# Performance work log

Hardware: AMD Instinct MI355X
Metric: run time of the kernel (lower is better)

Reference implementation:

```python
import jax, jax.numpy as jnp
import numpy as np

B, L, E, A, H = 1024, 200, 128, 128, 4

def setup_inputs() -> dict:
    key = jax.random.key(0)
    k1, k2, k3, k4, k5, k6 = jax.random.split(key, 6)
    inp = jax.random.normal(k1, (B, L, E), dtype=jnp.float32)
    mask = jax.random.randint(k2, (B, L), 0, 2).astype(bool)
    # guarantee at least one valid position per row (realistic: histories are non-empty)
    mask = mask.at[:, 0].set(True)
    pos_enc = jax.random.normal(k3, (1, L, E), dtype=jnp.float32)
    W1 = jax.random.normal(k4, (E, A), dtype=jnp.float32) / np.sqrt(E)
    W2 = jax.random.normal(k5, (A, H), dtype=jnp.float32) / np.sqrt(A)
    W_out = jax.random.normal(k6, (H * E, E), dtype=jnp.float32) / np.sqrt(H * E)
    return {"input": inp, "mask": mask, "pos_enc": pos_enc, "W1": W1, "W2": W2, "W_out": W_out}

def reference(input, mask, pos_enc, W1, W2, W_out):
    fm = mask.astype(input.dtype)[..., None]          # [B, L, 1]
    x = input * fm                                     # zero out padded positions
    xp = x + pos_enc                                   # broadcast [1, L, E]
    hidden = jnp.tanh(xp @ W1)                         # [B, L, A]
    att = hidden @ W2                                  # [B, L, H]
    att = jnp.swapaxes(att, 1, 2)                      # [B, H, L]
    neg = jnp.asarray(-(2.0 ** 32) + 1.0, dtype=att.dtype)
    att = jnp.where(mask[:, None, :], att, neg)
    att = jax.nn.softmax(att, axis=-1)                 # [B, H, L]
    pooled = jnp.einsum('bhl,ble->bhe', att, x)        # [B, H, E]
    flat = pooled.reshape(pooled.shape[0], -1)         # [B, H*E]
    return flat @ W_out                                # [B, E]
```

## Files before the change

kernel.cpp:

```cpp
#include <hip/hip_runtime.h>
#include <cfloat>

#define Bn 1024
#define Ln 200
#define En 128
#define An 128
#define Hn 4

#define WS_POSW1   0
#define WS_W1FRAG  106496
#define WS_ATTPOOL 139264
#define SLOT       1664
#define WS_WOUTT   1843200
#define WS_NEEDED  1974272

using f32x4  = __attribute__((ext_vector_type(4))) float;
using bf16x8 = __attribute__((ext_vector_type(8))) short;

__device__ __forceinline__ unsigned short f2bf(float f){
    unsigned u = __builtin_bit_cast(unsigned, f);
    u = (u + 0x7FFFu + ((u >> 16) & 1u)) >> 16;
    return (unsigned short)u;
}
__device__ __forceinline__ float bf2f(unsigned short s){
    unsigned u = ((unsigned)s) << 16;
    return __builtin_bit_cast(float, u);
}
__device__ __forceinline__ float tanh_cheap(float x){
    float e = __expf(2.f * x);
    float r = __builtin_amdgcn_rcpf(e + 1.f);
    return fmaf(-2.f, r, 1.f);
}
__device__ __forceinline__ float tanh_fast(float x){
    x = fminf(fmaxf(x, -12.f), 12.f);
    float e = __expf(2.f * x);
    return 1.f - 2.f / (e + 1.f);
}
__device__ __forceinline__ unsigned cvt_pk_bf16(float lo, float hi){
    unsigned r;
    asm("v_cvt_pk_bf16_f32 %0, %1, %2" : "=v"(r) : "v"(lo), "v"(hi));
    return r;
}
__device__ __forceinline__ int swz(int row, int k){
    return row * 128 + ((((k >> 3) ^ (row & 15)) << 3) | (k & 7));
}

__global__ __launch_bounds__(256) void sap_prep(
    const float* __restrict__ pos, const float* __restrict__ W1,
    const float* __restrict__ Wout, void* __restrict__ ws)
{
    const int t = threadIdx.x, blk = blockIdx.x;
    if (blk < 104){
        float* posW1 = (float*)((char*)ws + WS_POSW1);
        int l = blk * 2 + (t >> 7), a = t & 127;
        float acc = 0.f;
        if (l < Ln){
            #pragma unroll 4
            for (int k = 0; k < 128; ++k)
                acc += pos[l * En + k] * W1[k * An + a];
        }
        posW1[l * An + a] = acc;
    } else if (blk < 106){
        unsigned short* w1f = (unsigned short*)((char*)ws + WS_W1FRAG);
        int s = (blk - 104) * 256 + t;
        int lane = s & 63;
        int A = s >> 6;
        int c = lane & 15, q = lane >> 4;
        #pragma unroll
        for (int ks = 0; ks < 4; ++ks){
            unsigned short v[8];
            #pragma unroll
            for (int j = 0; j < 8; ++j)
                v[j] = f2bf(W1[(ks * 32 + q * 8 + j) * An + A * 16 + c]);
            *(bf16x8*)&w1f[(s * 4 + ks) * 8] = *(bf16x8*)v;
        }
    } else {
        unsigned short* wt = (unsigned short*)((char*)ws + WS_WOUTT);
        int flat = ((blk - 106) * 256 + t) * 4;
        int e = flat >> 9, k = flat & 511;
        unsigned short v[4];
        #pragma unroll
        for (int i = 0; i < 4; ++i)
            v[i] = f2bf(Wout[(size_t)(k + i) * En + e]);
        *(uint2*)&wt[flat] = *(uint2*)v;
    }
}

__global__ __launch_bounds__(512, 4) void sap_att10(
    const float* __restrict__ inp, const void* __restrict__ maskp,
    const float* __restrict__ W2, void* __restrict__ ws)
{
    __shared__ __align__(16) char smem_u[32768];
    __shared__ float s_att4[208 * 4];
    __shared__ float s_mask[256];

    unsigned short* s_x = (unsigned short*)smem_u;
    float (*s_part)[4][64] = (float (*)[4][64])(smem_u + 16384);
    float (*s_scr)[512]    = (float (*)[512])smem_u;

    const int t = threadIdx.x, lane = t & 63, w = t >> 6;
    const int c = lane & 15, q = lane >> 4;
    const int b = blockIdx.x;

    const unsigned short* w1f   = (const unsigned short*)((char*)ws + WS_W1FRAG);
    const float*          posW1 = (const float*)((char*)ws + WS_POSW1);
    unsigned short*       slot  = (unsigned short*)((char*)ws + WS_ATTPOOL + (size_t)b * SLOT);

    bf16x8 af[4];
    #pragma unroll
    for (int ks = 0; ks < 4; ++ks)
        af[ks] = *(const bf16x8*)&w1f[((w * 64 + lane) * 4 + ks) * 8];
    float4 w2a[4];
    #pragma unroll
    for (int v = 0; v < 4; ++v)
        w2a[v] = *(const float4*)&W2[(w * 16 + q * 4 + v) * Hn];

    {
        unsigned word = ((const unsigned*)maskp)[lane];
        unsigned long long bi  = __ballot(word > 1u);
        unsigned long long bfm = __ballot(word != 0u && word != 0x3F800000u);
        int flag = (bi == 0ull) ? 0 : ((bfm == 0ull) ? 2 : 1);
        if (t < 256){
            float m = 0.f;
            if (t < Ln){
                int mv;
                if (flag == 0)      mv = ((const int*)maskp)[b * Ln + t] != 0;
                else if (flag == 1) mv = ((const unsigned char*)maskp)[b * Ln + t] != 0;
                else                mv = ((const float*)maskp)[b * Ln + t] != 0.f;
                m = mv ? 1.f : 0.f;
            }
            s_mask[t] = m;
        }
    }

    for (int cch = 0; cch < 4; ++cch){
        const int NT = (cch < 3) ? 4 : 1;

        {
            const float4* in4 = (const float4*)(inp + (size_t)b * (Ln * En) + cch * 64 * En);
            #define PUTV(vi, idx) { int ll = (idx) >> 5, kk = ((idx) & 31) * 4;            \
                uint2 val = make_uint2(cvt_pk_bf16(vi.x, vi.y), cvt_pk_bf16(vi.z, vi.w));  \
                *(uint2*)&s_x[swz(ll, kk)] = val; }
            if (cch < 3){
                float4 u0 = in4[t], u1 = in4[t + 512], u2 = in4[t + 1024], u3 = in4[t + 1536];
                PUTV(u0, t) PUTV(u1, t + 512) PUTV(u2, t + 1024) PUTV(u3, t + 1536)
            } else {
                uint2 val = make_uint2(0u, 0u);
                if (t < 256){
                    float4 u0 = in4[t];
                    val = make_uint2(cvt_pk_bf16(u0.x, u0.y), cvt_pk_bf16(u0.z, u0.w));
                }
                int ll = t >> 5, kk = (t & 31) * 4;
                *(uint2*)&s_x[swz(ll, kk)] = val;
            }
            #undef PUTV
        }
        __syncthreads();

        for (int lt = 0; lt < NT; ++lt){
            int brow = lt * 16 + c;
            bf16x8 bfr[4];
            #pragma unroll
            for (int ks = 0; ks < 4; ++ks){
                int g = (ks * 4 + q) ^ c;
                bfr[ks] = *(bf16x8*)&s_x[brow * 128 + (g << 3)];
            }
            f32x4 acc = *(const f32x4*)&posW1[(size_t)(cch * 64 + brow) * An + w * 16 + q * 4];
            #pragma unroll
            for (int ks = 0; ks < 4; ++ks)
                acc = __builtin_amdgcn_mfma_f32_16x16x32_bf16(af[ks], bfr[ks], acc, 0, 0, 0);
            float contrib[4] = {0.f, 0.f, 0.f, 0.f};
            #pragma unroll
            for (int v = 0; v < 4; ++v){
                float hv = tanh_cheap(acc[v]);
                contrib[0] += hv * w2a[v].x;
                contrib[1] += hv * w2a[v].y;
                contrib[2] += hv * w2a[v].z;
                contrib[3] += hv * w2a[v].w;
            }
            #pragma unroll
            for (int h = 0; h < 4; ++h){
                contrib[h] += __shfl_xor(contrib[h], 16, 64);
                contrib[h] += __shfl_xor(contrib[h], 32, 64);
            }
            s_part[w][q][lt * 16 + c] = contrib[q];
        }
        __syncthreads();

        if (t < 256){
            int h = t >> 6, l = t & 63, gl = cch * 64 + l;
            if (gl < Ln){
                float a = 0.f;
                #pragma unroll
                for (int w2 = 0; w2 < 8; ++w2) a += s_part[w2][h][l];
                s_att4[gl * 4 + h] = (s_mask[gl] > 0.5f) ? a : -1.0e30f;
            }
        }
    }
    __syncthreads();

    if (t < 256){
        const int h = t >> 6, sl = t & 63;
        float v[4]; float mx = -FLT_MAX;
        #pragma unroll
        for (int i = 0; i < 4; ++i){
            int l = sl + i * 64;
            v[i] = (l < Ln) ? s_att4[l * 4 + h] : -3.0e38f;
            mx = fmaxf(mx, v[i]);
        }
        for (int s = 32; s; s >>= 1) mx = fmaxf(mx, __shfl_xor(mx, s, 64));
        float e[4]; float sum = 0.f;
        #pragma unroll
        for (int i = 0; i < 4; ++i){
            int l = sl + i * 64;
            e[i] = (l < Ln) ? __expf(v[i] - mx) : 0.f;
            sum += e[i];
        }
        for (int s = 32; s; s >>= 1) sum += __shfl_xor(sum, s, 64);
        float inv = 1.f / sum;
        #pragma unroll
        for (int i = 0; i < 4; ++i){
            int l = sl + i * 64;
            if (l < Ln) s_att4[l * 4 + h] = e[i] * inv;
        }
    }
    __syncthreads();

    {
        const int eg = t & 31, r = t >> 5;
        const float* xin = inp + (size_t)b * (Ln * En);
        f32x4 a0 = {0.f,0.f,0.f,0.f}, a1 = a0, a2 = a0, a3 = a0;
        for (int i = 0; i < 13; ++i){
            int l = i * 16 + r;
            if (l < Ln){
                f32x4 xv = *(const f32x4*)&xin[l * En + eg * 4];
                f32x4 w4 = *(const f32x4*)&s_att4[l * 4];
                a0 += xv * w4[0];
                a1 += xv * w4[1];
                a2 += xv * w4[2];
                a3 += xv * w4[3];
            }
        }
        *(f32x4*)&s_scr[r][0 * 128 + eg * 4] = a0;
        *(f32x4*)&s_scr[r][1 * 128 + eg * 4] = a1;
        *(f32x4*)&s_scr[r][2 * 128 + eg * 4] = a2;
        *(f32x4*)&s_scr[r][3 * 128 + eg * 4] = a3;
    }
    __syncthreads();

    {
        float sum = 0.f;
        #pragma unroll
        for (int r2 = 0; r2 < 16; ++r2) sum += s_scr[r2][t];
        slot[t] = f2bf(sum);
    }
}

__global__ __launch_bounds__(256) void sap_out(
    const void* __restrict__ ws, float* __restrict__ out)
{
    const unsigned short* wt = (const unsigned short*)((const char*)ws + WS_WOUTT);
    const int t = threadIdx.x, lane = t & 63, w = t >> 6;
    const int c = lane & 15, q = lane >> 4;
    const int b0 = blockIdx.x * 16;
    const int e0 = (blockIdx.y * 4 + w) * 16;

    const unsigned short* pslot =
        (const unsigned short*)((const char*)ws + WS_ATTPOOL + (size_t)(b0 + c) * SLOT);

    f32x4 acc = {0.f, 0.f, 0.f, 0.f};
    #pragma unroll 4
    for (int ks = 0; ks < 16; ++ks){
        bf16x8 afr = *(const bf16x8*)&pslot[ks * 32 + q * 8];
        bf16x8 bfr = *(const bf16x8*)&wt[(e0 + c) * 512 + ks * 32 + q * 8];
        acc = __builtin_amdgcn_mfma_f32_16x16x32_bf16(afr, bfr, acc, 0, 0, 0);
    }
    #pragma unroll
    for (int v = 0; v < 4; ++v)
        out[(size_t)(b0 + q * 4 + v) * En + e0 + c] = acc[v];
}

__global__ __launch_bounds__(512, 4) void sap_fused_v2(
    const float* __restrict__ inp, const void* __restrict__ maskp,
    const float* __restrict__ pos, const float* __restrict__ W1,
    const float* __restrict__ W2, const float* __restrict__ Wout,
    float* __restrict__ out)
{
#define LP 208
    __shared__ unsigned short s_xp [LP * 128];
    __shared__ float s_att [4 * LP];
    __shared__ float s_mask[LP];
    __shared__ float s_pool[512];
    __shared__ float s_red [512];
    __shared__ int   s_flag;

    const int t = threadIdx.x;
    const int b = blockIdx.x;
    const int lane = t & 63, w = t >> 6;
    const int c = lane & 15, q = lane >> 4;

    if (t == 0){
        const unsigned* mw = (const unsigned*)maskp;
        int fi = 1, ff = 1;
        for (int i = 0; i < 64; ++i){
            unsigned word = mw[i];
            if (word > 1u) fi = 0;
            if (word != 0u && word != 0x3F800000u) ff = 0;
        }
        s_flag = fi ? 0 : (ff ? 2 : 1);
    }
    bf16x8 af[4];
    {
        const int arow = w * 16 + c;
        #pragma unroll
        for (int ks = 0; ks < 4; ++ks)
            #pragma unroll
            for (int j = 0; j < 8; ++j)
                af[ks][j] = (short)f2bf(W1[(ks * 32 + q * 8 + j) * An + arow]);
    }
    float w2a[4][4];
    #pragma unroll
    for (int v = 0; v < 4; ++v){
        float4 wv = *(const float4*)&W2[(w * 16 + q * 4 + v) * Hn];
        w2a[v][0] = wv.x; w2a[v][1] = wv.y; w2a[v][2] = wv.z; w2a[v][3] = wv.w;
    }
    __syncthreads();
    const int flag = s_flag;
    for (int l = t; l < LP; l += 512){
        float m = 0.f;
        if (l < Ln){
            int mv;
            if (flag == 0)      mv = ((const int*)maskp)[b * Ln + l] != 0;
            else if (flag == 1) mv = ((const unsigned char*)maskp)[b * Ln + l] != 0;
            else                mv = ((const float*)maskp)[b * Ln + l] != 0.f;
            m = mv ? 1.f : 0.f;
        }
        s_mask[l] = m;
    }
    for (int i = t; i < 4 * LP; i += 512) s_att[i] = 0.f;
    __syncthreads();
    {
        const float4* in4 = (const float4*)(inp + (size_t)b * (Ln * En));
        const float4* p4  = (const float4*)pos;
        #pragma unroll
        for (int it = 0; it < 13; ++it){
            int idx = it * 512 + t;
            int l = idx >> 5;
            int k = (idx & 31) * 4;
            uint2 val;
            if (idx < 6400){
                float m = s_mask[l];
                float4 a = in4[idx];
                float4 p = p4[idx];
                val = make_uint2((unsigned)f2bf(a.x*m+p.x) | ((unsigned)f2bf(a.y*m+p.y) << 16),
                                 (unsigned)f2bf(a.z*m+p.z) | ((unsigned)f2bf(a.w*m+p.w) << 16));
            } else val = make_uint2(0u, 0u);
            *(uint2*)&s_xp[swz(l, k)] = val;
        }
    }
    __syncthreads();
    for (int lt = 0; lt < 13; ++lt){
        int brow = lt * 16 + c;
        bf16x8 bfr[4];
        #pragma unroll
        for (int ks = 0; ks < 4; ++ks){
            int g = (ks * 4 + q) ^ c;
            bfr[ks] = *(bf16x8*)&s_xp[brow * 128 + (g << 3)];
        }
        f32x4 acc = {0.f, 0.f, 0.f, 0.f};
        #pragma unroll
        for (int ks = 0; ks < 4; ++ks)
            acc = __builtin_amdgcn_mfma_f32_16x16x32_bf16(af[ks], bfr[ks], acc, 0, 0, 0);
        float hv[4];
        #pragma unroll
        for (int v = 0; v < 4; ++v) hv[v] = tanh_fast(acc[v]);
        #pragma unroll
        for (int h = 0; h < 4; ++h){
            float contrib = hv[0]*w2a[0][h] + hv[1]*w2a[1][h] + hv[2]*w2a[2][h] + hv[3]*w2a[3][h];
            contrib += __shfl_xor(contrib, 16, 64);
            contrib += __shfl_xor(contrib, 32, 64);
            if (lane < 16) atomicAdd(&s_att[h * LP + lt * 16 + lane], contrib);
        }
    }
    __syncthreads();
    if (t < 256){
        const int sl = t & 63, h = t >> 6;
        float v[4]; bool ok[4]; float mx = -FLT_MAX;
        #pragma unroll
        for (int i = 0; i < 4; ++i){
            int l = sl + i * 64;
            ok[i] = (l < Ln) && (s_mask[l] > 0.5f);
            v[i]  = ok[i] ? s_att[h * LP + l] : -FLT_MAX;
            mx = fmaxf(mx, v[i]);
        }
        for (int s = 32; s; s >>= 1) mx = fmaxf(mx, __shfl_xor(mx, s, 64));
        float e[4]; float sum = 0.f;
        #pragma unroll
        for (int i = 0; i < 4; ++i){ e[i] = ok[i] ? __expf(v[i]-mx) : 0.f; sum += e[i]; }
        for (int s = 32; s; s >>= 1) sum += __shfl_xor(sum, s, 64);
        float inv = 1.f / sum;
        #pragma unroll
        for (int i = 0; i < 4; ++i){ int l = sl + i*64; if (l < LP) s_att[h*LP+l] = e[i]*inv; }
    }
    __syncthreads();
    {
        int h = t >> 7, e = t & 127;
        float acc = 0.f;
        #pragma unroll 4
        for (int l = 0; l < Ln; ++l){
            float xv = bf2f(s_xp[swz(l, e)]) - pos[l * En + e];
            acc += s_att[h * LP + l] * xv;
        }
        s_pool[h * En + e] = acc;
    }
    __syncthreads();
    {
        int qt = t >> 7, e = t & 127;
        float acc = 0.f;
        const float* wo = Wout + (size_t)(qt * 128) * En + e;
        #pragma unroll 4
        for (int i = 0; i < 128; ++i)
            acc += s_pool[qt * 128 + i] * wo[(size_t)i * En];
        s_red[t] = acc;
    }
    __syncthreads();
    if (t < 128)
        out[(size_t)b * En + t] = s_red[t] + s_red[t + 128] + s_red[t + 256] + s_red[t + 384];
#undef LP
}

extern "C" void kernel_launch(void* const* d_in, const int* in_sizes, int n_in,
                              void* d_out, int out_size, void* d_ws, size_t ws_size,
                              hipStream_t stream)
{
    const float* inp  = (const float*)d_in[0];
    const void*  mask = d_in[1];
    const float* pos  = (const float*)d_in[2];
    const float* W1   = (const float*)d_in[3];
    const float* W2   = (const float*)d_in[4];
    const float* Wout = (const float*)d_in[5];
    float* out = (float*)d_out;

    if (ws_size >= WS_NEEDED){
        sap_prep<<<170, 256, 0, stream>>>(pos, W1, Wout, d_ws);
        sap_att10<<<Bn, 512, 0, stream>>>(inp, mask, W2, d_ws);
        sap_out<<<dim3(64, 2), 256, 0, stream>>>(d_ws, out);
    } else {
        sap_fused_v2<<<Bn, 512, 0, stream>>>(inp, mask, pos, W1, W2, Wout, out);
    }
}
```

Before: 64.46 us.

## Double-buffer input chunks in shared memory and accumulate attention scores with LDS atomics

```diff
diff --git a/kernel.cpp b/kernel.cpp
--- a/kernel.cpp
+++ b/kernel.cpp
@@ -86,7 +86,7 @@
     }
 }
 
-__global__ __launch_bounds__(512, 4) void sap_att10(
+__global__ __launch_bounds__(512, 4) void sap_att11(
     const float* __restrict__ inp, const void* __restrict__ maskp,
     const float* __restrict__ W2, void* __restrict__ ws)
 {
@@ -94,9 +94,7 @@
     __shared__ float s_att4[208 * 4];
     __shared__ float s_mask[256];
 
-    unsigned short* s_x = (unsigned short*)smem_u;
-    float (*s_part)[4][64] = (float (*)[4][64])(smem_u + 16384);
-    float (*s_scr)[512]    = (float (*)[512])smem_u;
+    float (*s_scr)[512] = (float (*)[512])smem_u;
 
     const int t = threadIdx.x, lane = t & 63, w = t >> 6;
     const int c = lane & 15, q = lane >> 4;
@@ -105,6 +103,7 @@
     const unsigned short* w1f   = (const unsigned short*)((char*)ws + WS_W1FRAG);
     const float*          posW1 = (const float*)((char*)ws + WS_POSW1);
     unsigned short*       slot  = (unsigned short*)((char*)ws + WS_ATTPOOL + (size_t)b * SLOT);
+    const float4*         in4   = (const float4*)(inp + (size_t)b * (Ln * En));
 
     bf16x8 af[4];
     #pragma unroll
@@ -114,6 +113,8 @@
     #pragma unroll
     for (int v = 0; v < 4; ++v)
         w2a[v] = *(const float4*)&W2[(w * 16 + q * 4 + v) * Hn];
+
+    for (int i = t; i < 832; i += 512) s_att4[i] = 0.f;
 
     {
         unsigned word = ((const unsigned*)maskp)[lane];
@@ -133,29 +134,32 @@
         }
     }
 
+    #define SXBUF(i) ((unsigned short*)(smem_u + (i) * 16384))
+    #define PUTV(sx, vi, idx) { int ll = (idx) >> 5, kk = ((idx) & 31) * 4;            \
+        uint2 val = make_uint2(cvt_pk_bf16(vi.x, vi.y), cvt_pk_bf16(vi.z, vi.w));      \
+        *(uint2*)&(sx)[swz(ll, kk)] = val; }
+
+    {
+        unsigned short* sx = SXBUF(0);
+        float4 u0 = in4[t], u1 = in4[t + 512], u2 = in4[t + 1024], u3 = in4[t + 1536];
+        PUTV(sx, u0, t) PUTV(sx, u1, t + 512) PUTV(sx, u2, t + 1024) PUTV(sx, u3, t + 1536)
+    }
+    __syncthreads();
+
     for (int cch = 0; cch < 4; ++cch){
+        const int cur = cch & 1;
         const int NT = (cch < 3) ? 4 : 1;
-
-        {
-            const float4* in4 = (const float4*)(inp + (size_t)b * (Ln * En) + cch * 64 * En);
-            #define PUTV(vi, idx) { int ll = (idx) >> 5, kk = ((idx) & 31) * 4;            \
-                uint2 val = make_uint2(cvt_pk_bf16(vi.x, vi.y), cvt_pk_bf16(vi.z, vi.w));  \
-                *(uint2*)&s_x[swz(ll, kk)] = val; }
-            if (cch < 3){
-                float4 u0 = in4[t], u1 = in4[t + 512], u2 = in4[t + 1024], u3 = in4[t + 1536];
-                PUTV(u0, t) PUTV(u1, t + 512) PUTV(u2, t + 1024) PUTV(u3, t + 1536)
-            } else {
-                uint2 val = make_uint2(0u, 0u);
-                if (t < 256){
-                    float4 u0 = in4[t];
-                    val = make_uint2(cvt_pk_bf16(u0.x, u0.y), cvt_pk_bf16(u0.z, u0.w));
-                }
-                int ll = t >> 5, kk = (t & 31) * 4;
-                *(uint2*)&s_x[swz(ll, kk)] = val;
-            }
-            #undef PUTV
-        }
-        __syncthreads();
+        unsigned short* s_x = SXBUF(cur);
+
+        const int nxt = cch + 1;
+        float4 u0 = make_float4(0.f,0.f,0.f,0.f), u1 = u0, u2 = u0, u3 = u0;
+        if (nxt < 3){
+            const int base = nxt * 2048;
+            u0 = in4[base + t];        u1 = in4[base + t + 512];
+            u2 = in4[base + t + 1024]; u3 = in4[base + t + 1536];
+        } else if (nxt == 3){
+            if (t < 256) u0 = in4[3 * 2048 + t];
+        }
 
         for (int lt = 0; lt < NT; ++lt){
             int brow = lt * 16 + c;
@@ -183,21 +187,28 @@
                 contrib[h] += __shfl_xor(contrib[h], 16, 64);
                 contrib[h] += __shfl_xor(contrib[h], 32, 64);
             }
-            s_part[w][q][lt * 16 + c] = contrib[q];
+            int gl = cch * 64 + brow;
+            if (gl < Ln)
+                atomicAdd(&s_att4[gl * 4 + q], contrib[q]);
+        }
+
+        if (nxt < 4){
+            unsigned short* s_n = SXBUF(cur ^ 1);
+            if (nxt < 3){
+                PUTV(s_n, u0, t) PUTV(s_n, u1, t + 512)
+                PUTV(s_n, u2, t + 1024) PUTV(s_n, u3, t + 1536)
+            } else {
+                uint2 val = make_uint2(0u, 0u);
+                if (t < 256)
+                    val = make_uint2(cvt_pk_bf16(u0.x, u0.y), cvt_pk_bf16(u0.z, u0.w));
+                int ll = t >> 5, kk = (t & 31) * 4;
+                *(uint2*)&s_n[swz(ll, kk)] = val;
+            }
         }
         __syncthreads();
-
-        if (t < 256){
-            int h = t >> 6, l = t & 63, gl = cch * 64 + l;
-            if (gl < Ln){
-                float a = 0.f;
-                #pragma unroll
-                for (int w2 = 0; w2 < 8; ++w2) a += s_part[w2][h][l];
-                s_att4[gl * 4 + h] = (s_mask[gl] > 0.5f) ? a : -1.0e30f;
-            }
-        }
-    }
-    __syncthreads();
+    }
+    #undef PUTV
+    #undef SXBUF
 
     if (t < 256){
         const int h = t >> 6, sl = t & 63;
@@ -205,7 +216,8 @@
         #pragma unroll
         for (int i = 0; i < 4; ++i){
             int l = sl + i * 64;
-            v[i] = (l < Ln) ? s_att4[l * 4 + h] : -3.0e38f;
+            v[i] = (l < Ln) ? ((s_mask[l] > 0.5f) ? s_att4[l * 4 + h] : -1.0e30f)
+                            : -3.0e38f;
             mx = fmaxf(mx, v[i]);
         }
         for (int s = 32; s; s >>= 1) mx = fmaxf(mx, __shfl_xor(mx, s, 64));
@@ -443,7 +455,7 @@
 
     if (ws_size >= WS_NEEDED){
         sap_prep<<<170, 256, 0, stream>>>(pos, W1, Wout, d_ws);
-        sap_att10<<<Bn, 512, 0, stream>>>(inp, mask, W2, d_ws);
+        sap_att11<<<Bn, 512, 0, stream>>>(inp, mask, W2, d_ws);
         sap_out<<<dim3(64, 2), 256, 0, stream>>>(d_ws, out);
     } else {
         sap_fused_v2<<<Bn, 512, 0, stream>>>(inp, mask, pos, W1, W2, Wout, out);
```

Measured after the change: 83.62 us. 29.7% more time.
